# Performance work log

Measured on AMD Instinct MI355X. Metric: run time of the kernel, lower is better.

The kernel has to match this reference:

```python
import jax, jax.numpy as jnp
import numpy as np

N_NODES = 50000
N_EDGES = 800000
N_GRAPHS = 512
IN_F = 128
HEADS = 8
HEAD_C = 8
OUT_F = HEADS * HEAD_C  # 64
NEG_SLOPE = 0.2


def setup_inputs() -> dict:
    key = jax.random.key(0)
    ks = jax.random.split(key, 10)
    x = jax.random.normal(ks[0], (N_NODES, IN_F), dtype=jnp.float32)
    edge_index = jax.random.randint(ks[1], (2, N_EDGES), 0, N_NODES, dtype=jnp.int64)
    batch = jnp.sort(jax.random.randint(ks[2], (N_NODES,), 0, N_GRAPHS, dtype=jnp.int64))
    s = 0.05
    W = jax.random.normal(ks[3], (IN_F, OUT_F), dtype=jnp.float32) * s
    att_src = jax.random.normal(ks[4], (HEADS, HEAD_C), dtype=jnp.float32) * s
    att_dst = jax.random.normal(ks[5], (HEADS, HEAD_C), dtype=jnp.float32) * s
    bias = jax.random.normal(ks[6], (OUT_F,), dtype=jnp.float32) * s
    pool_w_rel = jax.random.normal(ks[7], (OUT_F, 1), dtype=jnp.float32) * s
    pool_b_rel = jax.random.normal(ks[8], (1,), dtype=jnp.float32) * s
    pool_w_root = jax.random.normal(ks[9], (OUT_F, 1), dtype=jnp.float32) * s
    return {"x": x, "edge_index": edge_index, "batch": batch, "W": W,
            "att_src": att_src, "att_dst": att_dst, "bias": bias,
            "pool_w_rel": pool_w_rel, "pool_b_rel": pool_b_rel,
            "pool_w_root": pool_w_root}


def _segment_softmax(e, seg, num_segments):
    # numerically stable scatter-softmax over segments
    m = jax.ops.segment_max(e, seg, num_segments=num_segments)
    ex = jnp.exp(e - m[seg])
    denom = jax.ops.segment_sum(ex, seg, num_segments=num_segments)
    return ex / (denom[seg] + 1e-16)


def reference(x, edge_index, batch, W, att_src, att_dst, bias,
              pool_w_rel, pool_b_rel, pool_w_root):
    N = N_NODES
    # ---- GATConv (concat heads, self-loops added, LeakyReLU 0.2) ----
    loops = jnp.arange(N, dtype=edge_index.dtype)
    src = jnp.concatenate([edge_index[0], loops])
    dst = jnp.concatenate([edge_index[1], loops])
    h = (x @ W).reshape(N, HEADS, HEAD_C)                 # [N,H,C]
    a_s = jnp.einsum('nhc,hc->nh', h, att_src)            # [N,H]
    a_d = jnp.einsum('nhc,hc->nh', h, att_dst)
    e = jax.nn.leaky_relu(a_s[src] + a_d[dst], NEG_SLOPE) # [E+N,H]
    alpha = _segment_softmax(e, dst, N)                   # softmax over incoming edges
    out = jax.ops.segment_sum(h[src] * alpha[:, :, None], dst, num_segments=N)
    out = out.reshape(N, OUT_F) + bias                    # [N,64]
    # ---- SAGPooling(min_score=-1): GraphConv score + per-graph softmax,
    #      all nodes kept (softmax scores > -1), features scaled by score ----
    s2, d2 = edge_index[0], edge_index[1]
    aggr = jax.ops.segment_sum(out[s2], d2, num_segments=N)  # add-aggregation
    score = (aggr @ pool_w_rel + pool_b_rel + out @ pool_w_root)[:, 0]  # [N]
    score = _segment_softmax(score, batch, N_GRAPHS)
    att_x = out * score[:, None]
    # ---- global_add_pool ----
    g = jax.ops.segment_sum(att_x, batch, num_segments=N_GRAPHS)  # [G,64]
    return out, g
```

## Files before the change

### kernel.cpp

```cpp
#include <hip/hip_runtime.h>

#define NN 50000
#define NE 800000
#define NG 512
#define INF_ 128
#define OUTF 64
#define CAP 64

#define NPB 98
#define BSHIFT 9
#define BNODES 512
#define BCAP 9216
#define NCHUNK 250
#define BCH 3200

#define GEMM_BLOCKS ((NN + 63) / 64)
#define FRONT_BLOCKS 1032

#define XSTRIDE 136

__device__ __forceinline__ unsigned short f2bf(float f) {
    unsigned int u = __float_as_uint(f);
    unsigned int r = (u + 0x7fffu + ((u >> 16) & 1u)) >> 16;
    return (unsigned short)r;
}
__device__ __forceinline__ float bf2f(unsigned int lo16) {
    return __uint_as_float(lo16 << 16);
}

__global__ __launch_bounds__(256) void k_front(
    const int* __restrict__ ei, int* __restrict__ bcnt,
    unsigned int* __restrict__ ebuf, float* __restrict__ gden,
    float* __restrict__ g_num,
    const float* __restrict__ x, const float* __restrict__ W,
    const float* __restrict__ att_src, const float* __restrict__ att_dst,
    unsigned short* __restrict__ hb, float* __restrict__ a_s,
    float* __restrict__ a_d)
{
    __shared__ union {
        struct {
            unsigned short Ws[INF_ * OUTF];
            unsigned short Xs[64 * XSTRIDE];
        } g;
        struct {
            int hist[128];
            int bofs[128];
            int goff[128];
            unsigned int pk[BCH];
            unsigned int ord[BCH];
        } b;
    } sm;

    {
        int idx = blockIdx.x * 256 + threadIdx.x;
        if (idx < NG) gden[idx] = 0.f;
        else if (idx < NG + NG * OUTF) g_num[idx - NG] = 0.f;
    }

    const int t = threadIdx.x;
    int gemmIdx;
    if (blockIdx.x < 1000) {
        const int oct = blockIdx.x >> 2;
        const int r   = blockIdx.x & 3;
        if (r == 0) {
            if (t < 128) sm.b.hist[t] = 0;
            __syncthreads();

            const int e0 = oct * BCH;
            for (int i = t; i < BCH; i += 256) {
                int e = e0 + i;
                int s = ei[e];
                int d = ei[NE + e];
                int bb = d >> BSHIFT;
                unsigned int v = ((unsigned int)bb << 25) |
                                 ((unsigned int)(d & (BNODES - 1)) << 16) |
                                 (unsigned int)s;
                sm.b.pk[i] = v;
                atomicAdd(&sm.b.hist[bb], 1);
            }
            __syncthreads();

            int cntv = 0;
            if (t < 128) {
                cntv = sm.b.hist[t];
                sm.b.bofs[t] = cntv;
                sm.b.goff[t] = (t < NPB) ? atomicAdd(&bcnt[t], cntv) : 0;
            }
            __syncthreads();
            for (int off = 1; off < 128; off <<= 1) {
                int v2;
                if (t < 128) {
                    v2 = sm.b.bofs[t];
                    if (t >= off) v2 += sm.b.bofs[t - off];
                }
                __syncthreads();
                if (t < 128) sm.b.bofs[t] = v2;
                __syncthreads();
            }
            if (t < 128) {
                int excl = sm.b.bofs[t] - cntv;
                sm.b.bofs[t] = excl;
                sm.b.hist[t] = excl;
            }
            __syncthreads();

            for (int i = t; i < BCH; i += 256) {
                unsigned int v = sm.b.pk[i];
                int bb = v >> 25;
                int p = atomicAdd(&sm.b.hist[bb], 1);
                sm.b.ord[p] = v;
            }
            __syncthreads();

            for (int i = t; i < BCH; i += 256) {
                unsigned int v = sm.b.ord[i];
                int bb = v >> 25;
                int gp = sm.b.goff[bb] + (i - sm.b.bofs[bb]);
                if (gp < BCAP) ebuf[(size_t)bb * BCAP + gp] = v;
            }
            return;
        }
        gemmIdx = oct * 3 + (r - 1);
    } else {
        gemmIdx = 750 + (blockIdx.x - 1000);
    }

    const int n0 = gemmIdx * 64;

    #pragma unroll
    for (int it = 0; it < 8; it++) {
        int i = it * 256 + threadIdx.x;
        float4 v = ((const float4*)W)[i];
        ushort4 b;
        b.x = f2bf(v.x); b.y = f2bf(v.y); b.z = f2bf(v.z); b.w = f2bf(v.w);
        ((ushort4*)sm.g.Ws)[i] = b;
    }

    #pragma unroll
    for (int it = 0; it < 8; it++) {
        int idx = it * 256 + threadIdx.x;
        int row = idx >> 5;
        int c4  = idx & 31;
        int n = n0 + row;
        if (n > NN - 1) n = NN - 1;
        float4 v = ((const float4*)(x + (size_t)n * INF_))[c4];
        ushort4 b;
        b.x = f2bf(v.x); b.y = f2bf(v.y); b.z = f2bf(v.z); b.w = f2bf(v.w);
        *(ushort4*)&sm.g.Xs[row * XSTRIDE + c4 * 4] = b;
    }
    __syncthreads();

    const int colg = threadIdx.x & 15;
    const int rowg = threadIdx.x >> 4;

    const unsigned short* xr[4];
    #pragma unroll
    for (int rr = 0; rr < 4; rr++)
        xr[rr] = &sm.g.Xs[(rowg * 4 + rr) * XSTRIDE];

    float acc[4][4];
    #pragma unroll
    for (int rr = 0; rr < 4; rr++)
        #pragma unroll
        for (int c = 0; c < 4; c++) acc[rr][c] = 0.f;

    for (int k8 = 0; k8 < INF_ / 8; k8++) {
        uint4 xv[4];
        #pragma unroll
        for (int rr = 0; rr < 4; rr++)
            xv[rr] = *(const uint4*)(xr[rr] + k8 * 8);
        #pragma unroll
        for (int kk = 0; kk < 8; kk++) {
            uint2 wu = *(const uint2*)&sm.g.Ws[(k8 * 8 + kk) * OUTF + colg * 4];
            float w0 = bf2f(wu.x & 0xffffu), w1 = bf2f(wu.x >> 16);
            float w2 = bf2f(wu.y & 0xffffu), w3 = bf2f(wu.y >> 16);
            #pragma unroll
            for (int rr = 0; rr < 4; rr++) {
                unsigned int pair = ((const unsigned int*)&xv[rr])[kk >> 1];
                float xs_ = bf2f((kk & 1) ? (pair >> 16) : (pair & 0xffffu));
                acc[rr][0] = fmaf(xs_, w0, acc[rr][0]);
                acc[rr][1] = fmaf(xs_, w1, acc[rr][1]);
                acc[rr][2] = fmaf(xs_, w2, acc[rr][2]);
                acc[rr][3] = fmaf(xs_, w3, acc[rr][3]);
            }
        }
    }

    float asv[4], adv[4];
    #pragma unroll
    for (int c = 0; c < 4; c++) {
        asv[c] = att_src[colg * 4 + c];
        adv[c] = att_dst[colg * 4 + c];
    }

    #pragma unroll
    for (int rr = 0; rr < 4; rr++) {
        const int n = n0 + rowg * 4 + rr;
        const bool valid = (n < NN);
        if (valid) {
            ushort4 o;
            o.x = f2bf(acc[rr][0]); o.y = f2bf(acc[rr][1]);
            o.z = f2bf(acc[rr][2]); o.w = f2bf(acc[rr][3]);
            ((ushort4*)(hb + (size_t)n * OUTF))[colg] = o;
        }
        float vs = acc[rr][0]*asv[0] + acc[rr][1]*asv[1] + acc[rr][2]*asv[2] + acc[rr][3]*asv[3];
        float vd = acc[rr][0]*adv[0] + acc[rr][1]*adv[1] + acc[rr][2]*adv[2] + acc[rr][3]*adv[3];
        vs += __shfl_xor(vs, 1, 64);
        vd += __shfl_xor(vd, 1, 64);
        if (valid && !(colg & 1)) {
            a_s[n * 8 + (colg >> 1)] = vs;
            a_d[n * 8 + (colg >> 1)] = vd;
        }
    }
}

#define BHALF 256
__global__ __launch_bounds__(256) void k_build(
    const unsigned int* __restrict__ ebuf, const int* __restrict__ bcnt,
    int* __restrict__ deg, unsigned short* __restrict__ adj)
{
    __shared__ unsigned short ladj[BHALF * CAP];
    __shared__ int ldeg[BHALF];

    const int b    = blockIdx.x >> 1;
    const int half = blockIdx.x & 1;
    const int rlo  = half * BHALF;
    const int t    = threadIdx.x;

    if (t < BHALF) ldeg[t] = 0;
    __syncthreads();

    const int cnt = min(bcnt[b], BCAP);
    const unsigned int* eb = ebuf + (size_t)b * BCAP;
    for (int i = t; i < cnt; i += 256) {
        unsigned int v = eb[i];
        int drel = (v >> 16) & (BNODES - 1);
        unsigned int rr = (unsigned int)(drel - rlo);
        if (rr < BHALF) {
            int p = atomicAdd(&ldeg[rr], 1);
            if (p < CAP) ladj[rr * CAP + p] = (unsigned short)(v & 0xffffu);
        }
    }
    __syncthreads();

    const int n0 = b * BNODES + rlo;
    if (t < BHALF) {
        int n = n0 + t;
        if (n < NN) deg[n] = ldeg[t];
    }
    for (int i = t; i < BHALF * CAP / 8; i += 256) {
        int n = n0 + (i >> 3);
        if (n < NN)
            ((uint4*)(adj + (size_t)n * CAP))[i & 7] = ((const uint4*)ladj)[i];
    }
}

__global__ __launch_bounds__(256) void k_aggr(
    const unsigned short* __restrict__ hb, const float* __restrict__ a_s,
    const float* __restrict__ a_d, const int* __restrict__ deg,
    const unsigned short* __restrict__ adj, const float* __restrict__ bias,
    const float* __restrict__ w_rel, const float* __restrict__ w_root,
    float* __restrict__ out, float* __restrict__ t_rel, float* __restrict__ t_root)
{
    const int wid  = threadIdx.x >> 6;
    const int lane = threadIdx.x & 63;
    const int g    = lane >> 3;
    const int c8   = lane & 7;
    const int n    = blockIdx.x * 4 + wid;
    if (n >= NN) return;

    const float ad_n = a_d[n * 8 + c8];

    float acc[8];
    #pragma unroll
    for (int k = 0; k < 8; k++) acc[k] = 0.f;
    float den = 0.f;

    if (g == 0) {
        float e0 = a_s[n * 8 + c8] + ad_n;
        e0 = e0 > 0.f ? e0 : 0.2f * e0;
        float ex0 = __expf(e0);
        uint4 hv = *(const uint4*)(hb + (size_t)n * OUTF + c8 * 8);
        acc[0] = ex0 * bf2f(hv.x & 0xffffu); acc[1] = ex0 * bf2f(hv.x >> 16);
        acc[2] = ex0 * bf2f(hv.y & 0xffffu); acc[3] = ex0 * bf2f(hv.y >> 16);
        acc[4] = ex0 * bf2f(hv.z & 0xffffu); acc[5] = ex0 * bf2f(hv.z >> 16);
        acc[6] = ex0 * bf2f(hv.w & 0xffffu); acc[7] = ex0 * bf2f(hv.w >> 16);
        den = ex0;
    }

    const int cnt = min(deg[n], CAP);
    const unsigned short* lst = adj + (size_t)n * CAP;
    for (int i = g; i < cnt; i += 8) {
        int s = lst[i];
        float as = a_s[s * 8 + c8];
        uint4 hv = *(const uint4*)(hb + (size_t)s * OUTF + c8 * 8);
        float e = as + ad_n;
        e = e > 0.f ? e : 0.2f * e;
        float ex = __expf(e);
        acc[0] = fmaf(ex, bf2f(hv.x & 0xffffu), acc[0]);
        acc[1] = fmaf(ex, bf2f(hv.x >> 16),     acc[1]);
        acc[2] = fmaf(ex, bf2f(hv.y & 0xffffu), acc[2]);
        acc[3] = fmaf(ex, bf2f(hv.y >> 16),     acc[3]);
        acc[4] = fmaf(ex, bf2f(hv.z & 0xffffu), acc[4]);
        acc[5] = fmaf(ex, bf2f(hv.z >> 16),     acc[5]);
        acc[6] = fmaf(ex, bf2f(hv.w & 0xffffu), acc[6]);
        acc[7] = fmaf(ex, bf2f(hv.w >> 16),     acc[7]);
        den += ex;
    }

    #pragma unroll
    for (int m = 8; m < 64; m <<= 1) {
        den += __shfl_xor(den, m, 64);
        #pragma unroll
        for (int k = 0; k < 8; k++) acc[k] += __shfl_xor(acc[k], m, 64);
    }

    const float inv = 1.f / (den + 1e-16f);
    float o[8];
    #pragma unroll
    for (int k = 0; k < 8; k++) o[k] = acc[k] * inv + bias[c8 * 8 + k];

    if (g == 0) {
        float4 o0 = make_float4(o[0], o[1], o[2], o[3]);
        float4 o1 = make_float4(o[4], o[5], o[6], o[7]);
        float4* op = (float4*)(out + (size_t)n * OUTF + c8 * 8);
        op[0] = o0; op[1] = o1;
    }

    float vr = 0.f, vt = 0.f;
    #pragma unroll
    for (int k = 0; k < 8; k++) {
        vr = fmaf(o[k], w_rel[c8 * 8 + k], vr);
        vt = fmaf(o[k], w_root[c8 * 8 + k], vt);
    }
    #pragma unroll
    for (int m = 1; m < 8; m <<= 1) {
        vr += __shfl_xor(vr, m, 64);
        vt += __shfl_xor(vt, m, 64);
    }
    if (lane == 0) { t_rel[n] = vr; t_root[n] = vt; }
}

__global__ __launch_bounds__(256) void k_score_pool(
    const int* __restrict__ deg, const unsigned short* __restrict__ adj,
    const float* __restrict__ t_rel, const float* __restrict__ t_root,
    const float* __restrict__ pool_b, const int* __restrict__ batch,
    const float* __restrict__ out,
    float* __restrict__ gden, float* __restrict__ g_num)
{
    __shared__ float ex_s[32];
    __shared__ int   b_s[32];

    const int wid  = threadIdx.x >> 6;
    const int lane = threadIdx.x & 63;
    const int sub  = lane >> 3;
    const int g    = lane & 7;
    const int base_n = blockIdx.x * 32;
    const int n    = base_n + wid * 8 + sub;

    const int cnt = (n < NN) ? min(deg[n], CAP) : 0;
    const unsigned short* lst = adj + (size_t)n * CAP;
    float acc = 0.f;
    for (int i = g; i < cnt; i += 8) acc += t_rel[lst[i]];
    #pragma unroll
    for (int m = 1; m < 8; m <<= 1) acc += __shfl_xor(acc, m, 64);

    if (g == 0) {
        const int slot = wid * 8 + sub;
        if (n < NN) {
            float ex = __expf(acc + t_root[n] + pool_b[0]);
            ex_s[slot] = ex;
            b_s[slot]  = batch[n];
        } else {
            ex_s[slot] = 0.f;
            b_s[slot]  = -1;
        }
    }
    __syncthreads();

    if (threadIdx.x == 0) {
        float racc = 0.f;
        int bcur = -1;
        for (int i = 0; i < 32; i++) {
            int b = b_s[i];
            if (b != bcur) {
                if (bcur >= 0) atomicAdd(&gden[bcur], racc);
                bcur = b; racc = 0.f;
            }
            racc += ex_s[i];
        }
        if (bcur >= 0) atomicAdd(&gden[bcur], racc);
    }

    const int j = lane;
    float facc = 0.f;
    int bcur = -1;
    for (int i = 0; i < 8; i++) {
        const int slot = wid * 8 + i;
        const int n2 = base_n + slot;
        if (n2 >= NN) break;
        int b = b_s[slot];
        if (b != bcur) {
            if (bcur >= 0) atomicAdd(&g_num[bcur * OUTF + j], facc);
            bcur = b; facc = 0.f;
        }
        facc = fmaf(out[(size_t)n2 * OUTF + j], ex_s[slot], facc);
    }
    if (bcur >= 0) atomicAdd(&g_num[bcur * OUTF + j], facc);
}

__global__ __launch_bounds__(256) void k_gfinal(
    const float* __restrict__ g_num, const float* __restrict__ gden,
    float* __restrict__ g)
{
    int i = blockIdx.x * 256 + threadIdx.x;
    if (i < NG * OUTF) g[i] = g_num[i] / (gden[i >> 6] + 1e-16f);
}

extern "C" void kernel_launch(void* const* d_in, const int* in_sizes, int n_in,
                              void* d_out, int out_size, void* d_ws, size_t ws_size,
                              hipStream_t stream)
{
    const float* x        = (const float*)d_in[0];
    const int*   ei       = (const int*)  d_in[1];
    const int*   batch    = (const int*)  d_in[2];
    const float* W        = (const float*)d_in[3];
    const float* att_src  = (const float*)d_in[4];
    const float* att_dst  = (const float*)d_in[5];
    const float* bias     = (const float*)d_in[6];
    const float* w_rel    = (const float*)d_in[7];
    const float* pool_b   = (const float*)d_in[8];
    const float* w_root   = (const float*)d_in[9];

    float* out_nodes = (float*)d_out;
    float* g_out     = (float*)d_out + (size_t)NN * OUTF;

    char* base = (char*)d_ws;
    unsigned short* hb = (unsigned short*)(base);
    float* a_s       = (float*)(base +  6400000);
    float* a_d       = (float*)(base +  8000000);
    float* t_rel     = (float*)(base +  9600000);
    float* t_root    = (float*)(base +  9800000);
    float* gden      = (float*)(base + 10000000);
    float* g_num     = (float*)(base + 10002048);
    int*   deg       = (int*)  (base + 10133120);
    unsigned short* adjl = (unsigned short*)(base + 10333120);
    unsigned int* ebuf = (unsigned int*)(base + 16733120);
    int*   bcnt      = (int*)  (base + 20345792);

    hipMemsetAsync(bcnt, 0, 512, stream);

    k_front<<<FRONT_BLOCKS, 256, 0, stream>>>(
        ei, bcnt, ebuf, gden, g_num,
        x, W, att_src, att_dst, hb, a_s, a_d);
    k_build<<<NPB * 2, 256, 0, stream>>>(ebuf, bcnt, deg, adjl);
    k_aggr<<<(NN + 3) / 4, 256, 0, stream>>>(hb, a_s, a_d, deg, adjl, bias,
                                             w_rel, w_root, out_nodes, t_rel, t_root);
    k_score_pool<<<(NN + 31) / 32, 256, 0, stream>>>(deg, adjl, t_rel, t_root,
                                                     pool_b, batch, out_nodes,
                                                     gden, g_num);
    k_gfinal<<<(NG * OUTF + 255) / 256, 256, 0, stream>>>(g_num, gden, g_out);
}
```

Measured before the change: 173.6 us.

## Use bf16 MFMA for node projection GEMM and batch neighbor gathers

Replaces the scalar FMA projection x@W in the front kernel with MFMA 16x16x32 bf16 instructions. W is stored transposed in shared memory, and the attention dot products are reduced with lane shuffles. Separately, the GAT aggregation loop issues its first four neighbor loads up front so the gathers are in flight together and their memory latency overlaps. The cost is transposed scalar LDS writes and extra register use for the prefetched values.

```diff
diff --git a/kernel.cpp b/kernel.cpp
--- a/kernel.cpp
+++ b/kernel.cpp
@@ -27,6 +27,9 @@
 __device__ __forceinline__ float bf2f(unsigned int lo16) {
     return __uint_as_float(lo16 << 16);
 }
+
+using bf16x8 = __attribute__((ext_vector_type(8))) __bf16;
+using f32x4  = __attribute__((ext_vector_type(4))) float;
 
 __global__ __launch_bounds__(256) void k_front(
     const int* __restrict__ ei, int* __restrict__ bcnt,
@@ -39,7 +42,7 @@
 {
     __shared__ union {
         struct {
-            unsigned short Ws[INF_ * OUTF];
+            unsigned short Wt[OUTF * XSTRIDE];
             unsigned short Xs[64 * XSTRIDE];
         } g;
         struct {
@@ -129,16 +132,19 @@
 
     #pragma unroll
     for (int it = 0; it < 8; it++) {
-        int i = it * 256 + threadIdx.x;
+        int i = it * 256 + t;
+        int k  = i >> 4;
+        int n4 = (i & 15) * 4;
         float4 v = ((const float4*)W)[i];
-        ushort4 b;
-        b.x = f2bf(v.x); b.y = f2bf(v.y); b.z = f2bf(v.z); b.w = f2bf(v.w);
-        ((ushort4*)sm.g.Ws)[i] = b;
+        sm.g.Wt[(n4 + 0) * XSTRIDE + k] = f2bf(v.x);
+        sm.g.Wt[(n4 + 1) * XSTRIDE + k] = f2bf(v.y);
+        sm.g.Wt[(n4 + 2) * XSTRIDE + k] = f2bf(v.z);
+        sm.g.Wt[(n4 + 3) * XSTRIDE + k] = f2bf(v.w);
     }
 
     #pragma unroll
     for (int it = 0; it < 8; it++) {
-        int idx = it * 256 + threadIdx.x;
+        int idx = it * 256 + t;
         int row = idx >> 5;
         int c4  = idx & 31;
         int n = n0 + row;
@@ -150,66 +156,67 @@
     }
     __syncthreads();
 
-    const int colg = threadIdx.x & 15;
-    const int rowg = threadIdx.x >> 4;
-
-    const unsigned short* xr[4];
-    #pragma unroll
-    for (int rr = 0; rr < 4; rr++)
-        xr[rr] = &sm.g.Xs[(rowg * 4 + rr) * XSTRIDE];
-
-    float acc[4][4];
-    #pragma unroll
-    for (int rr = 0; rr < 4; rr++)
+    const int lane = t & 63;
+    const int w    = t >> 6;
+    const int q    = lane & 15;
+    const int h4   = lane >> 4;
+
+    f32x4 acc[4];
+    #pragma unroll
+    for (int ct = 0; ct < 4; ct++) acc[ct] = (f32x4){0.f, 0.f, 0.f, 0.f};
+
+    const unsigned short* Ax = &sm.g.Xs[(w * 16 + q) * XSTRIDE + h4 * 8];
+    const unsigned short* Bw = &sm.g.Wt[q * XSTRIDE + h4 * 8];
+
+    #pragma unroll
+    for (int ks = 0; ks < 4; ks++) {
+        bf16x8 av = *(const bf16x8*)(Ax + ks * 32);
         #pragma unroll
-        for (int c = 0; c < 4; c++) acc[rr][c] = 0.f;
-
-    for (int k8 = 0; k8 < INF_ / 8; k8++) {
-        uint4 xv[4];
-        #pragma unroll
-        for (int rr = 0; rr < 4; rr++)
-            xv[rr] = *(const uint4*)(xr[rr] + k8 * 8);
-        #pragma unroll
-        for (int kk = 0; kk < 8; kk++) {
-            uint2 wu = *(const uint2*)&sm.g.Ws[(k8 * 8 + kk) * OUTF + colg * 4];
-            float w0 = bf2f(wu.x & 0xffffu), w1 = bf2f(wu.x >> 16);
-            float w2 = bf2f(wu.y & 0xffffu), w3 = bf2f(wu.y >> 16);
-            #pragma unroll
-            for (int rr = 0; rr < 4; rr++) {
-                unsigned int pair = ((const unsigned int*)&xv[rr])[kk >> 1];
-                float xs_ = bf2f((kk & 1) ? (pair >> 16) : (pair & 0xffffu));
-                acc[rr][0] = fmaf(xs_, w0, acc[rr][0]);
-                acc[rr][1] = fmaf(xs_, w1, acc[rr][1]);
-                acc[rr][2] = fmaf(xs_, w2, acc[rr][2]);
-                acc[rr][3] = fmaf(xs_, w3, acc[rr][3]);
-            }
-        }
-    }
-
-    float asv[4], adv[4];
-    #pragma unroll
-    for (int c = 0; c < 4; c++) {
-        asv[c] = att_src[colg * 4 + c];
-        adv[c] = att_dst[colg * 4 + c];
-    }
-
-    #pragma unroll
-    for (int rr = 0; rr < 4; rr++) {
-        const int n = n0 + rowg * 4 + rr;
+        for (int ct = 0; ct < 4; ct++) {
+            bf16x8 bv = *(const bf16x8*)(Bw + ct * 16 * XSTRIDE + ks * 32);
+            acc[ct] = __builtin_amdgcn_mfma_f32_16x16x32_bf16(av, bv, acc[ct], 0, 0, 0);
+        }
+    }
+
+    float atts[4], attd[4];
+    #pragma unroll
+    for (int ct = 0; ct < 4; ct++) {
+        int head = 2 * ct + (q >> 3);
+        atts[ct] = att_src[head * 8 + (q & 7)];
+        attd[ct] = att_dst[head * 8 + (q & 7)];
+    }
+
+    #pragma unroll
+    for (int r = 0; r < 4; r++) {
+        const int n = n0 + w * 16 + h4 * 4 + r;
         const bool valid = (n < NN);
         if (valid) {
-            ushort4 o;
-            o.x = f2bf(acc[rr][0]); o.y = f2bf(acc[rr][1]);
-            o.z = f2bf(acc[rr][2]); o.w = f2bf(acc[rr][3]);
-            ((ushort4*)(hb + (size_t)n * OUTF))[colg] = o;
-        }
-        float vs = acc[rr][0]*asv[0] + acc[rr][1]*asv[1] + acc[rr][2]*asv[2] + acc[rr][3]*asv[3];
-        float vd = acc[rr][0]*adv[0] + acc[rr][1]*adv[1] + acc[rr][2]*adv[2] + acc[rr][3]*adv[3];
-        vs += __shfl_xor(vs, 1, 64);
-        vd += __shfl_xor(vd, 1, 64);
-        if (valid && !(colg & 1)) {
-            a_s[n * 8 + (colg >> 1)] = vs;
-            a_d[n * 8 + (colg >> 1)] = vd;
+            #pragma unroll
+            for (int ct = 0; ct < 4; ct++)
+                hb[(size_t)n * OUTF + ct * 16 + q] = f2bf(acc[ct][r]);
+        }
+        float ps[4], pd[4];
+        #pragma unroll
+        for (int ct = 0; ct < 4; ct++) {
+            float v = acc[ct][r];
+            ps[ct] = v * atts[ct];
+            pd[ct] = v * attd[ct];
+        }
+        #pragma unroll
+        for (int m = 1; m < 8; m <<= 1) {
+            #pragma unroll
+            for (int ct = 0; ct < 4; ct++) {
+                ps[ct] += __shfl_xor(ps[ct], m, 64);
+                pd[ct] += __shfl_xor(pd[ct], m, 64);
+            }
+        }
+        if (valid && (q & 7) == 0) {
+            #pragma unroll
+            for (int ct = 0; ct < 4; ct++) {
+                int head = 2 * ct + (q >> 3);
+                a_s[n * 8 + head] = ps[ct];
+                a_d[n * 8 + head] = pd[ct];
+            }
         }
     }
 }
@@ -290,7 +297,37 @@
 
     const int cnt = min(deg[n], CAP);
     const unsigned short* lst = adj + (size_t)n * CAP;
-    for (int i = g; i < cnt; i += 8) {
+
+    int sv[4];
+    #pragma unroll
+    for (int ii = 0; ii < 4; ii++) {
+        int i = g + ii * 8;
+        sv[ii] = (i < cnt) ? (int)lst[i] : -1;
+    }
+    float asl[4]; uint4 hvl[4];
+    #pragma unroll
+    for (int ii = 0; ii < 4; ii++) {
+        int s = (sv[ii] >= 0) ? sv[ii] : n;
+        asl[ii] = a_s[s * 8 + c8];
+        hvl[ii] = *(const uint4*)(hb + (size_t)s * OUTF + c8 * 8);
+    }
+    #pragma unroll
+    for (int ii = 0; ii < 4; ii++) {
+        float e = asl[ii] + ad_n;
+        e = e > 0.f ? e : 0.2f * e;
+        float ex = (sv[ii] >= 0) ? __expf(e) : 0.f;
+        uint4 hv = hvl[ii];
+        acc[0] = fmaf(ex, bf2f(hv.x & 0xffffu), acc[0]);
+        acc[1] = fmaf(ex, bf2f(hv.x >> 16),     acc[1]);
+        acc[2] = fmaf(ex, bf2f(hv.y & 0xffffu), acc[2]);
+        acc[3] = fmaf(ex, bf2f(hv.y >> 16),     acc[3]);
+        acc[4] = fmaf(ex, bf2f(hv.z & 0xffffu), acc[4]);
+        acc[5] = fmaf(ex, bf2f(hv.z >> 16),     acc[5]);
+        acc[6] = fmaf(ex, bf2f(hv.w & 0xffffu), acc[6]);
+        acc[7] = fmaf(ex, bf2f(hv.w >> 16),     acc[7]);
+        den += ex;
+    }
+    for (int i = g + 32; i < cnt; i += 8) {
         int s = lst[i];
         float as = a_s[s * 8 + c8];
         uint4 hv = *(const uint4*)(hb + (size_t)s * OUTF + c8 * 8);
```

Result: faster. 162.0 us (median of 2 runs) (-6.7%).
